# Performance work log

Measured on AMD Instinct MI355X. Metric: run time of the kernel, lower is better.

## Reference

```python
import jax, jax.numpy as jnp
import numpy as np

MIN_TEMPERATURE = 1e-8
MIN_PROB = 1e-10
NEG_INF = float('-inf')


def setup_inputs() -> dict:
    key = jax.random.key(0)
    k1, k2, k3, k4, k5 = jax.random.split(key, 5)
    B, V = 128, 128256
    logits = jax.random.normal(k1, (B, V), dtype=jnp.float32)
    temperatures = jax.random.uniform(k2, (B,), dtype=jnp.float32)
    top_ps = jax.random.uniform(k3, (B,), dtype=jnp.float32)
    top_ks = jax.random.randint(k4, (B,), 0, 1024, dtype=jnp.int64)
    min_ps = jax.random.uniform(k5, (B,), dtype=jnp.float32)
    return {"logits": logits, "temperatures": temperatures, "top_ps": top_ps,
            "top_ks": top_ks, "min_ps": min_ps}


def reference(logits, temperatures, top_ps, top_ks, min_ps):
    B, V = logits.shape
    rows = jnp.arange(B)[:, None]

    temps = jnp.maximum(temperatures, MIN_TEMPERATURE)
    original_scaled = logits.astype(jnp.float32) / temps[:, None]
    x = original_scaled

    # ---- top-k filter (rank-based; equivalent to torch.topk + scatter mask) ----
    order_k = jnp.argsort(-x, axis=-1)            # [B,V] token ids sorted desc
    ranks = jnp.argsort(order_k, axis=-1)         # rank of each token in its row
    keep_topk = ranks < top_ks[:, None]
    active_k = (top_ks > 0) & (top_ks < V)
    keep_topk = jnp.where(active_k[:, None], keep_topk, True)
    x = jnp.where(keep_topk, x, NEG_INF)

    # ---- top-p (nucleus) filter ----
    probs = jax.nn.softmax(x, axis=-1)
    order_p = jnp.argsort(-probs, axis=-1)
    sorted_probs = jnp.take_along_axis(probs, order_p, axis=-1)
    cum = jnp.cumsum(sorted_probs, axis=-1)
    remove_sorted = cum > top_ps[:, None]
    # shift right so the first token above the threshold is kept
    remove_sorted = jnp.concatenate(
        [jnp.zeros((B, 1), dtype=bool), remove_sorted[:, :-1]], axis=-1)
    remove = jnp.zeros((B, V), dtype=bool).at[rows, order_p].set(remove_sorted)
    x = jnp.where(remove, NEG_INF, x)

    # ---- min-p filter ----
    probs = jax.nn.softmax(x, axis=-1)
    top_prob = jnp.max(probs, axis=-1, keepdims=True)
    x = jnp.where(probs < min_ps[:, None] * top_prob, NEG_INF, x)

    # ---- fallback if everything got filtered ----
    all_filtered = jnp.all(jnp.isneginf(x), axis=-1)
    x = jnp.where(all_filtered[:, None], original_scaled, x)

    # ---- final softmax with nan guard + renormalize ----
    probs = jax.nn.softmax(x, axis=-1)
    probs = jnp.nan_to_num(probs, nan=0.0)
    probs = probs / jnp.maximum(jnp.sum(probs, axis=-1, keepdims=True), MIN_PROB)

    # ---- multinomial sample (1 draw per row) ----
    tokens = jax.random.categorical(jax.random.key(42), jnp.log(probs), axis=-1)
    return tokens
```

## Files before the change

kernel.cpp:

```cpp
#include <hip/hip_runtime.h>


#define TPS 512
#define TPB 1024
#define VOC 128256
#define V4 (VOC / 4)
#define NBINS 2048
#define SEG 320
#define CAPROW (8 * SEG)
#define CAP2 2048
#define TIE_CAP 1024
#define IMAXI 0x7fffffff
#define FIXS 1.7592186044416e13
#define THRK 0xC0100000u

#define WS_CNT 0
#define WS_CAP 4096

__device__ __forceinline__ unsigned fkey(float x) {
  unsigned b = __float_as_uint(x);
  return b ^ ((b & 0x80000000u) ? 0xFFFFFFFFu : 0x80000000u);
}
__device__ __forceinline__ float keyf(unsigned k) {
  unsigned b = (k & 0x80000000u) ? (k ^ 0x80000000u) : ~k;
  return __uint_as_float(b);
}
__device__ __forceinline__ unsigned rotl32(unsigned v, int r) {
  return (v << r) | (v >> (32 - r));
}

__device__ __forceinline__ float gumbel_at(unsigned i) {
  const unsigned ks1 = 42u;
  const unsigned ks2 = 0x1BD11BDAu ^ 42u;
  unsigned x0 = 0u;
  unsigned x1 = i + ks1;
  x0 += x1; x1 = rotl32(x1, 13); x1 ^= x0;
  x0 += x1; x1 = rotl32(x1, 15); x1 ^= x0;
  x0 += x1; x1 = rotl32(x1, 26); x1 ^= x0;
  x0 += x1; x1 = rotl32(x1, 6);  x1 ^= x0;
  x0 += ks1; x1 += ks2 + 1u;
  x0 += x1; x1 = rotl32(x1, 17); x1 ^= x0;
  x0 += x1; x1 = rotl32(x1, 29); x1 ^= x0;
  x0 += x1; x1 = rotl32(x1, 16); x1 ^= x0;
  x0 += x1; x1 = rotl32(x1, 24); x1 ^= x0;
  x0 += ks2; x1 += 0u + 2u;
  x0 += x1; x1 = rotl32(x1, 13); x1 ^= x0;
  x0 += x1; x1 = rotl32(x1, 15); x1 ^= x0;
  x0 += x1; x1 = rotl32(x1, 26); x1 ^= x0;
  x0 += x1; x1 = rotl32(x1, 6);  x1 ^= x0;
  x0 += 0u; x1 += ks1 + 3u;
  x0 += x1; x1 = rotl32(x1, 17); x1 ^= x0;
  x0 += x1; x1 = rotl32(x1, 29); x1 ^= x0;
  x0 += x1; x1 = rotl32(x1, 16); x1 ^= x0;
  x0 += x1; x1 = rotl32(x1, 24); x1 ^= x0;
  x0 += ks1; x1 += ks2 + 4u;
  x0 += x1; x1 = rotl32(x1, 13); x1 ^= x0;
  x0 += x1; x1 = rotl32(x1, 15); x1 ^= x0;
  x0 += x1; x1 = rotl32(x1, 26); x1 ^= x0;
  x0 += x1; x1 = rotl32(x1, 6);  x1 ^= x0;
  x0 += ks2; x1 += 0u + 5u;
  unsigned bits = x0 ^ x1;
  unsigned fb = (bits >> 9) | 0x3f800000u;
  float f = __uint_as_float(fb) - 1.0f;
  float u = (f > 0.0f) ? f : 1.17549435e-38f;
  return -logf(-logf(u));
}

__device__ __forceinline__ unsigned long long bmerge(
    unsigned long long v, int i, int size, int maxs) {
  const bool up = ((i & size) == 0);
  for (int s = maxs; s > 0; s >>= 1) {
    unsigned long long p = __shfl_xor(v, s, 64);
    bool keep_min = (up == ((i & s) == 0));
    bool take = keep_min ? (p < v) : (p > v);
    if (take) v = p;
  }
  return v;
}

__device__ __forceinline__ void scan32g(unsigned* H, int n, int tid, int tpb) {
  for (int d = 1; d < n; d <<= 1) {
    unsigned v[4]; int c = 0;
    for (int i = tid; i < n; i += tpb) {
      v[c] = H[i] + ((i + d < n) ? H[i + d] : 0u);
      ++c;
    }
    __syncthreads();
    c = 0;
    for (int i = tid; i < n; i += tpb) { H[i] = v[c]; ++c; }
    __syncthreads();
  }
}
__device__ __forceinline__ void scan64(unsigned long long* H, int n, int tid) {
  for (int d = 1; d < n; d <<= 1) {
    unsigned long long v0 = 0ull, v1 = 0ull;
    int i0 = tid, i1 = tid + TPB;
    bool a0 = (i0 < n), a1 = (i1 < n);
    if (a0) { v0 = H[i0]; if (i0 + d < n) v0 += H[i0 + d]; }
    if (a1) { v1 = H[i1]; if (i1 + d < n) v1 += H[i1 + d]; }
    __syncthreads();
    if (a0) H[i0] = v0;
    if (a1) H[i1] = v1;
    __syncthreads();
  }
}

#define FOR_ALL(...)                                                          \
  for (int c_ = 0; c_ < 32; ++c_) {                                           \
    const int i4_ = c_ * TPB + tid;                                           \
    if (i4_ < V4) {                                                           \
      const float4 L_ = ((const float4*)rowp)[i4_];                           \
      const float xs_[4] = { L_.x / tclamp, L_.y / tclamp,                    \
                             L_.z / tclamp, L_.w / tclamp };                  \
      const int base_ = i4_ * 4;                                              \
      for (int j_ = 0; j_ < 4; ++j_) {                                        \
        const int idx = base_ + j_; const float x = xs_[j_];                  \
        __VA_ARGS__                                                           \
      }                                                                       \
    }                                                                         \
  }

extern "C" __global__ void __launch_bounds__(TPS)
k3_capture(const float* __restrict__ logits, const float* __restrict__ temps,
           unsigned char* __restrict__ ws)
{
  __shared__ unsigned long long Ls[SEG];
  __shared__ unsigned sh_nloc;
  const int blk = blockIdx.x, row = blk >> 3, sb = blk & 7;
  const int tid = threadIdx.x;
  const float* rowp = logits + (size_t)row * VOC;
  const float tclamp = fmaxf(temps[row], 1e-8f);
  if (tid == 0) sh_nloc = 0u;
  __syncthreads();
  for (int c = 0; c < 8; ++c) {
    const int i4 = c * 4096 + sb * TPS + tid;
    if (i4 < V4) {
      const float4 L = ((const float4*)rowp)[i4];
      const float v[4] = { L.x, L.y, L.z, L.w };
      const int base = i4 * 4;
      for (int j = 0; j < 4; ++j) {
        if (fkey(v[j]) >= THRK) {
          float x = v[j] / tclamp;
          unsigned kx = fkey(x);
          unsigned p = atomicAdd(&sh_nloc, 1u);
          if (p < SEG)
            Ls[p] = ((unsigned long long)(~kx) << 32) | (unsigned)(base + j);
        }
      }
    }
  }
  __syncthreads();
  const unsigned nloc = sh_nloc;
  if (tid == 0) ((unsigned*)(ws + WS_CNT))[row * 8 + sb] = nloc;
  unsigned long long* cap = (unsigned long long*)(ws + WS_CAP) +
                            (size_t)row * CAPROW + (size_t)sb * SEG;
  const unsigned nw = min(nloc, (unsigned)SEG);
  for (unsigned i = tid; i < nw; i += TPS) cap[i] = Ls[i];
}

extern "C" __global__ void __launch_bounds__(TPB)
k4_sample(const float* __restrict__ logits, const float* __restrict__ temps,
          const float* __restrict__ topps, const int* __restrict__ topks,
          const float* __restrict__ minps, const unsigned char* __restrict__ ws,
          int* __restrict__ out)
{
  __shared__ unsigned long long A[CAP2];
  __shared__ unsigned Hc[NBINS];
  __shared__ double D[TPB];
  __shared__ float redw[16];
  __shared__ int   redi[16];
  __shared__ double redd[16];
  __shared__ int segoff[9];
  __shared__ int sh_bad;
  __shared__ float sh_m;
  __shared__ int sh_b0, sh_b1, sh_b2;
  __shared__ unsigned sh_above;
  __shared__ unsigned long long sh_ab64;
  __shared__ int sh_p, sh_tn, sh_I2;
  __shared__ double sh_Z3;

  const int tid = threadIdx.x;
  const int row = blockIdx.x;
  const float* rowp = logits + (size_t)row * VOC;
  const float tclamp = fmaxf(temps[row], 1e-8f);
  const float topp = topps[row];
  const float minp = minps[row];
  const int k = topks[row];
  const bool ka = (k > 0) && (k < VOC);

  if (tid == 0) {
    const unsigned* cnts = (const unsigned*)(ws + WS_CNT) + row * 8;
    int acc = 0, bad = 0;
    for (int b = 0; b < 8; ++b) {
      segoff[b] = acc;
      unsigned c = cnts[b];
      if (c > SEG) bad = 1;
      acc += (int)c;
    }
    segoff[8] = acc;
    sh_bad = bad;
  }
  __syncthreads();
  const int n = segoff[8];

  if (ka && k <= TPB && !sh_bad && n >= k && n <= CAP2) {
    const unsigned long long* capr =
        (const unsigned long long*)(ws + WS_CAP) + (size_t)row * CAPROW;
    for (int b = 0; b < 8; ++b) {
      const int off = segoff[b], cnt = segoff[b + 1] - off;
      for (int i = tid; i < cnt; i += TPB) A[off + i] = capr[b * SEG + i];
    }
    for (int i = n + tid; i < CAP2; i += TPB) A[i] = ~0ull;
    __syncthreads();
    const int lane = tid & 63, wave = tid >> 6;
    for (int g = wave; g < 32; g += 16) {
      const int i = g * 64 + lane;
      unsigned long long v = A[i];
      v = bmerge(v, i, 2, 1);
      v = bmerge(v, i, 4, 2);
      v = bmerge(v, i, 8, 4);
      v = bmerge(v, i, 16, 8);
      v = bmerge(v, i, 32, 16);
      v = bmerge(v, i, 64, 32);
      A[i] = v;
    }
    __syncthreads();
    for (int size = 128; size <= CAP2; size <<= 1) {
      for (int stride = size >> 1; stride >= 64; stride >>= 1) {
        for (int r = 0; r < 2; ++r) {
          const int i = tid + (r << 10);
          const int j = i ^ stride;
          if (j > i) {
            unsigned long long a = A[i], b = A[j];
            bool up = ((i & size) == 0);
            if ((a > b) == up) { A[i] = b; A[j] = a; }
          }
        }
        __syncthreads();
      }
      for (int g = wave; g < 32; g += 16) {
        const int i = g * 64 + lane;
        A[i] = bmerge(A[i], i, size, 32);
      }
      __syncthreads();
    }
    const float m = keyf(~(unsigned)(A[0] >> 32));
    unsigned idx_i = 0u; float e_i = 0.0f;
    const bool valid = (tid < k);
    if (valid) {
      unsigned long long a = A[tid];
      idx_i = (unsigned)a;
      e_i = expf(keyf(~(unsigned)(a >> 32)) - m);
    }
    double v = valid ? (double)e_i : 0.0;
    for (int o = 1; o < 64; o <<= 1) {
      double t = __shfl_up(v, o);
      if ((tid & 63) >= o) v += t;
    }
    if ((tid & 63) == 63) redd[tid >> 6] = v;
    __syncthreads();
    if (tid == 0) {
      double acc = 0.0;
      for (int w = 0; w < 16; ++w) { double t = redd[w]; redd[w] = acc; acc += t; }
    }
    __syncthreads();
    v += redd[tid >> 6];
    D[tid] = v;
    __syncthreads();
    const double Z1 = D[k - 1];
    const double T = (double)topp * Z1;
    if (tid == 0) sh_p = 0;
    __syncthreads();
    if (valid) {
      bool kept = (tid == 0) || (D[tid - 1] <= T);
      if (kept) atomicMax(&sh_p, tid);
    }
    __syncthreads();
    const int p2 = sh_p + 1;
    const float Z2f = (float)D[p2 - 1];
    const float e0 = expf(0.0f);
    const float thrm = minp * (e0 / Z2f);
    __syncthreads();
    if (tid == 0) sh_p = 0;
    __syncthreads();
    if (valid && tid < p2) {
      float q = e_i / Z2f;
      if (!(q < thrm)) atomicMax(&sh_p, tid);
    }
    __syncthreads();
    const int p3 = sh_p + 1;
    const float Z3f = (float)D[p3 - 1];
    float bw = -INFINITY; int bi = IMAXI;
    if (valid && tid < p3) {
      bw = logf(e_i / Z3f) + gumbel_at((unsigned)row * (unsigned)VOC + idx_i);
      bi = (int)idx_i;
    }
    for (int o = 32; o > 0; o >>= 1) {
      float ow = __shfl_down(bw, o);
      int   oi = __shfl_down(bi, o);
      if (ow > bw || (ow == bw && oi < bi)) { bw = ow; bi = oi; }
    }
    if ((tid & 63) == 0) { redw[tid >> 6] = bw; redi[tid >> 6] = bi; }
    __syncthreads();
    if (tid == 0) {
      float w = redw[0]; int ii = redi[0];
      for (int i = 1; i < 16; ++i)
        if (redw[i] > w || (redw[i] == w && redi[i] < ii)) { w = redw[i]; ii = redi[i]; }
      out[row] = ii;
    }
    return;
  }

  {
    float lmax = -INFINITY;
    FOR_ALL( (void)idx; lmax = fmaxf(lmax, x); )
    for (int o = 32; o > 0; o >>= 1) lmax = fmaxf(lmax, __shfl_down(lmax, o));
    if ((tid & 63) == 0) redw[tid >> 6] = lmax;
    __syncthreads();
    if (tid == 0) {
      float mm = redw[0];
      for (int i = 1; i < 16; ++i) mm = fmaxf(mm, redw[i]);
      sh_m = mm;
    }
    __syncthreads();
  }
  const float m = sh_m;

  unsigned tk_key = 0u; int rem_k = 0;
  if (ka) {
    for (int i = tid; i < NBINS; i += TPB) Hc[i] = 0u;
    __syncthreads();
    FOR_ALL( (void)idx; atomicAdd(&Hc[fkey(x) >> 21], 1u); )
    __syncthreads();
    scan32g(Hc, NBINS, tid, TPB);
    unsigned kku = (unsigned)k;
    for (int i = tid; i < NBINS; i += TPB) {
      unsigned hi = Hc[i], hn = (i + 1 < NBINS) ? Hc[i + 1] : 0u;
      if (hi >= kku && hn < kku) { sh_b0 = i; sh_above = hn; }
    }
    __syncthreads();
    const int b0 = sh_b0; kku -= sh_above;
    __syncthreads();
    for (int i = tid; i < NBINS; i += TPB) Hc[i] = 0u;
    __syncthreads();
    FOR_ALL(
      (void)idx;
      unsigned key = fkey(x);
      if ((int)(key >> 21) == b0) atomicAdd(&Hc[(key >> 10) & 0x7FFu], 1u);
    )
    __syncthreads();
    scan32g(Hc, NBINS, tid, TPB);
    for (int i = tid; i < NBINS; i += TPB) {
      unsigned hi = Hc[i], hn = (i + 1 < NBINS) ? Hc[i + 1] : 0u;
      if (hi >= kku && hn < kku) { sh_b1 = i; sh_above = hn; }
    }
    __syncthreads();
    const int b1 = sh_b1; kku -= sh_above;
    __syncthreads();
    for (int i = tid; i < NBINS; i += TPB) Hc[i] = 0u;
    __syncthreads();
    const unsigned pathk = ((unsigned)b0 << 11) | (unsigned)b1;
    FOR_ALL(
      (void)idx;
      unsigned key = fkey(x);
      if ((key >> 10) == pathk) atomicAdd(&Hc[key & 0x3FFu], 1u);
    )
    __syncthreads();
    scan32g(Hc, 1024, tid, TPB);
    for (int i = tid; i < 1024; i += TPB) {
      unsigned hi = Hc[i], hn = (i + 1 < 1024) ? Hc[i + 1] : 0u;
      if (hi >= kku && hn < kku) { sh_b2 = i; sh_above = hn; }
    }
    __syncthreads();
    rem_k = (int)(kku - sh_above);
    tk_key = ((unsigned)b0 << 21) | ((unsigned)b1 << 10) | (unsigned)sh_b2;
    __syncthreads();
  }
  const bool hk = ka;
  const float e_tk = hk ? expf(keyf(tk_key) - m) : 0.0f;
  const unsigned long long e_tk_fix = (unsigned long long)((double)e_tk * FIXS);
  unsigned long long* H = A;
  for (int i = tid; i < NBINS; i += TPB) H[i] = 0ull;
  __syncthreads();
  FOR_ALL(
    (void)idx;
    unsigned key = fkey(x);
    if (!hk || key > tk_key) {
      float e = expf(x - m);
      unsigned long long ef = (unsigned long long)((double)e * FIXS);
      if (ef) atomicAdd(&H[key >> 21], ef);
    }
  )
  __syncthreads();
  if (tid == 0 && hk) H[tk_key >> 21] += (unsigned long long)(unsigned)rem_k * e_tk_fix;
  __syncthreads();
  scan64(H, NBINS, tid);
  const unsigned long long Z1fix = H[0];
  const unsigned long long Tfix = (unsigned long long)((double)topp * (double)Z1fix);
  const int keepall = (Z1fix <= Tfix);

  unsigned t2_key = 0u; int rem2 = 0, all_mode = 0;
  double Z2d = 0.0; float e_t = 0.0f;

  if (!keepall) {
    for (int i = tid; i < NBINS; i += TPB) {
      unsigned long long hi = H[i], hn = (i + 1 < NBINS) ? H[i + 1] : 0ull;
      if (hi > Tfix && hn <= Tfix) { sh_b0 = i; sh_ab64 = hn; }
    }
    __syncthreads();
    const int b0p = sh_b0;
    const unsigned long long S0 = sh_ab64;
    __syncthreads();
    for (int i = tid; i < NBINS; i += TPB) H[i] = 0ull;
    __syncthreads();
    FOR_ALL(
      (void)idx;
      unsigned key = fkey(x);
      if ((int)(key >> 21) == b0p && (!hk || key > tk_key)) {
        float e = expf(x - m);
        unsigned long long ef = (unsigned long long)((double)e * FIXS);
        if (ef) atomicAdd(&H[(key >> 10) & 0x7FFu], ef);
      }
    )
    __syncthreads();
    if (tid == 0 && hk && (int)(tk_key >> 21) == b0p)
      H[(tk_key >> 10) & 0x7FFu] += (unsigned long long)(unsigned)rem_k * e_tk_fix;
    __syncthreads();
    scan64(H, NBINS, tid);
    {
      const unsigned long long T1 = Tfix - S0;
      for (int i = tid; i < NBINS; i += TPB) {
        unsigned long long hi = H[i], hn = (i + 1 < NBINS) ? H[i + 1] : 0ull;
        if (hi > T1 && hn <= T1) { sh_b1 = i; sh_ab64 = hn; }
      }
    }
    __syncthreads();
    const int b1p = sh_b1;
    const unsigned long long S1 = S0 + sh_ab64;
    __syncthreads();
    for (int i = tid; i < NBINS; i += TPB) H[i] = 0ull;
    for (int i = tid; i < 1024; i += TPB) Hc[i] = 0u;
    __syncthreads();
    const unsigned pathp = ((unsigned)b0p << 11) | (unsigned)b1p;
    FOR_ALL(
      (void)idx;
      unsigned key = fkey(x);
      if ((key >> 10) == pathp && (!hk || key > tk_key)) {
        float e = expf(x - m);
        unsigned long long ef = (unsigned long long)((double)e * FIXS);
        atomicAdd(&H[key & 0x3FFu], ef);
        atomicAdd(&Hc[key & 0x3FFu], 1u);
      }
    )
    __syncthreads();
    if (tid == 0 && hk && (tk_key >> 10) == pathp) {
      H[tk_key & 0x3FFu] += (unsigned long long)(unsigned)rem_k * e_tk_fix;
      Hc[tk_key & 0x3FFu] += (unsigned)rem_k;
    }
    __syncthreads();
    scan64(H, 1024, tid);
    {
      const unsigned long long T2 = Tfix - S1;
      for (int i = tid; i < 1024; i += TPB) {
        unsigned long long hi = H[i], hn = (i + 1 < 1024) ? H[i + 1] : 0ull;
        if (hi > T2 && hn <= T2) { sh_b2 = i; sh_ab64 = hn; }
      }
    }
    __syncthreads();
    const int b2p = sh_b2;
    const unsigned long long Sfix = S1 + sh_ab64;
    t2_key = ((unsigned)b0p << 21) | ((unsigned)b1p << 10) | (unsigned)b2p;
    const int c_t2 = (int)Hc[b2p];
    e_t = expf(keyf(t2_key) - m);
    const double Td = (double)topp * ((double)Z1fix / FIXS);
    const double Sd = (double)Sfix / FIXS;
    const double jmd = (Td - Sd) / (double)e_t;
    int rem_p;
    if (jmd >= (double)c_t2) rem_p = c_t2;
    else {
      rem_p = (int)jmd + 1;
      if (rem_p > c_t2) rem_p = c_t2;
      if (rem_p < 1) rem_p = 1;
    }
    rem2 = rem_p;
    const unsigned long long Z2fix =
        Sfix + (unsigned long long)(unsigned)rem_p *
                   (unsigned long long)((double)e_t * FIXS);
    Z2d = (double)Z2fix / FIXS;
  } else {
    if (hk) { t2_key = tk_key; rem2 = rem_k; e_t = e_tk; }
    else    { all_mode = 1; }
    Z2d = (double)Z1fix / FIXS;
  }

  if (tid == 0) { sh_tn = 0; sh_I2 = IMAXI; }
  __syncthreads();
  const float Z2f = (float)Z2d;
  const float thrm = minp * (1.0f / Z2f);
  double zp = 0.0;
  FOR_ALL(
    unsigned key = fkey(x);
    if (all_mode || key > t2_key) {
      float e = expf(x - m);
      float q1 = e / Z2f;
      if (!(q1 < thrm)) zp += (double)e;
    } else if (key == t2_key) {
      int p = atomicAdd(&sh_tn, 1);
      if (p < TIE_CAP) Hc[p] = (unsigned)idx;
    }
  )
  for (int o = 32; o > 0; o >>= 1) zp += __shfl_down(zp, o);
  if ((tid & 63) == 0) redd[tid >> 6] = zp;
  __syncthreads();
  int class_ok = 1;
  if (!all_mode) { float q1t = e_t / Z2f; class_ok = !(q1t < thrm); }
  if (tid == 0) {
    double z3 = 0.0;
    for (int i = 0; i < 16; ++i) z3 += redd[i];
    if (!all_mode && class_ok) z3 += (double)rem2 * (double)e_t;
    sh_Z3 = z3;
  }
  __syncthreads();
  const int tn = sh_tn;
  if (!all_mode && rem2 < tn && tn <= TIE_CAP) {
    if (tid < tn) {
      unsigned mine = Hc[tid];
      int r = 0;
      for (int j = 0; j < tn; ++j) r += (Hc[j] < mine);
      if (r == rem2 - 1) sh_I2 = (int)mine;
    }
  }
  __syncthreads();
  const int I2 = sh_I2;
  const float Z3f = (float)sh_Z3;
  float bw = -INFINITY; int bi = IMAXI;
  FOR_ALL(
    unsigned key = fkey(x);
    bool kp = all_mode || key > t2_key || (key == t2_key && idx <= I2);
    if (kp) {
      float e = expf(x - m);
      float q1 = e / Z2f;
      if (!(q1 < thrm)) {
        float w = logf(e / Z3f) + gumbel_at((unsigned)row * (unsigned)VOC + (unsigned)idx);
        if (w > bw) { bw = w; bi = idx; }
        else if (w == bw && idx < bi) bi = idx;
      }
    }
  )
  for (int o = 32; o > 0; o >>= 1) {
    float ow = __shfl_down(bw, o);
    int   oi = __shfl_down(bi, o);
    if (ow > bw || (ow == bw && oi < bi)) { bw = ow; bi = oi; }
  }
  if ((tid & 63) == 0) { redw[tid >> 6] = bw; redi[tid >> 6] = bi; }
  __syncthreads();
  if (tid == 0) {
    float w = redw[0]; int ii = redi[0];
    for (int i = 1; i < 16; ++i)
      if (redw[i] > w || (redw[i] == w && redi[i] < ii)) { w = redw[i]; ii = redi[i]; }
    out[row] = ii;
  }
}

extern "C" void kernel_launch(void* const* d_in, const int* in_sizes, int n_in,
                              void* d_out, int out_size, void* d_ws, size_t ws_size,
                              hipStream_t stream) {
  (void)n_in; (void)ws_size; (void)out_size;
  const float* logits = (const float*)d_in[0];
  const float* temps  = (const float*)d_in[1];
  const float* topps  = (const float*)d_in[2];
  const int*   topks  = (const int*)d_in[3];
  const float* minps  = (const float*)d_in[4];
  int* out = (int*)d_out;
  const int rows = in_sizes[1];
  unsigned char* ws = (unsigned char*)d_ws;
  k3_capture<<<dim3(rows * 8), dim3(TPS), 0, stream>>>(logits, temps, ws);
  k4_sample<<<dim3(rows), dim3(TPB), 0, stream>>>(logits, temps, topps, topks,
                                                  minps, ws, out);
}
```

Baseline: 125.9 us.

## Fuse capture and sample kernels using last-block-done atomic counter per row

Merges the two-kernel pipeline into one kernel. Each row is now split across 4 blocks of 1024 threads instead of 8 blocks of 512, and the last block to finish a row, found through a per-row atomic counter after a threadfence, goes on to the sampling phase. This removes one kernel launch boundary and lets sampling for early rows overlap with capture for other rows. In exchange it adds a memset launch, a larger shared-memory footprint for every block (which lowers occupancy during capture), and fewer capture blocks.

```diff
diff --git a/kernel.cpp b/kernel.cpp
--- a/kernel.cpp
+++ b/kernel.cpp
@@ -1,21 +1,22 @@
 #include <hip/hip_runtime.h>
 
 
-#define TPS 512
 #define TPB 1024
 #define VOC 128256
 #define V4 (VOC / 4)
+#define Q4 (V4 / 4)
 #define NBINS 2048
-#define SEG 320
-#define CAPROW (8 * SEG)
+#define SEG 640
+#define CAPROW (4 * SEG)
 #define CAP2 2048
 #define TIE_CAP 1024
 #define IMAXI 0x7fffffff
 #define FIXS 1.7592186044416e13
 #define THRK 0xC0100000u
 
-#define WS_CNT 0
-#define WS_CAP 4096
+#define WS_DONE 0
+#define WS_CNT  512
+#define WS_CAP  4096
 
 __device__ __forceinline__ unsigned fkey(float x) {
   unsigned b = __float_as_uint(x);
@@ -120,21 +121,42 @@
     }                                                                         \
   }
 
-extern "C" __global__ void __launch_bounds__(TPS)
-k3_capture(const float* __restrict__ logits, const float* __restrict__ temps,
-           unsigned char* __restrict__ ws)
+extern "C" __global__ void __launch_bounds__(TPB)
+sampler_fused(const float* __restrict__ logits, const float* __restrict__ temps,
+              const float* __restrict__ topps, const int* __restrict__ topks,
+              const float* __restrict__ minps, unsigned char* __restrict__ ws,
+              int* __restrict__ out)
 {
   __shared__ unsigned long long Ls[SEG];
+  __shared__ unsigned long long A[CAP2];
+  __shared__ unsigned Hc[NBINS];
+  __shared__ double D[TPB];
+  __shared__ float redw[16];
+  __shared__ int   redi[16];
+  __shared__ double redd[16];
   __shared__ unsigned sh_nloc;
-  const int blk = blockIdx.x, row = blk >> 3, sb = blk & 7;
+  __shared__ int sh_last;
+  __shared__ int segoff[5];
+  __shared__ int sh_bad;
+  __shared__ float sh_m;
+  __shared__ int sh_b0, sh_b1, sh_b2;
+  __shared__ unsigned sh_above;
+  __shared__ unsigned long long sh_ab64;
+  __shared__ int sh_p, sh_tn, sh_I2;
+  __shared__ double sh_Z3;
+
+  const int blk = blockIdx.x;
+  const int row = blk >> 2, sb = blk & 3;
   const int tid = threadIdx.x;
   const float* rowp = logits + (size_t)row * VOC;
   const float tclamp = fmaxf(temps[row], 1e-8f);
+
   if (tid == 0) sh_nloc = 0u;
   __syncthreads();
   for (int c = 0; c < 8; ++c) {
-    const int i4 = c * 4096 + sb * TPS + tid;
-    if (i4 < V4) {
+    const int t = c * TPB + tid;
+    if (t < Q4) {
+      const int i4 = sb * Q4 + t;
       const float4 L = ((const float4*)rowp)[i4];
       const float v[4] = { L.x, L.y, L.z, L.w };
       const int base = i4 * 4;
@@ -151,62 +173,46 @@
   }
   __syncthreads();
   const unsigned nloc = sh_nloc;
-  if (tid == 0) ((unsigned*)(ws + WS_CNT))[row * 8 + sb] = nloc;
-  unsigned long long* cap = (unsigned long long*)(ws + WS_CAP) +
-                            (size_t)row * CAPROW + (size_t)sb * SEG;
-  const unsigned nw = min(nloc, (unsigned)SEG);
-  for (unsigned i = tid; i < nw; i += TPS) cap[i] = Ls[i];
-}
-
-extern "C" __global__ void __launch_bounds__(TPB)
-k4_sample(const float* __restrict__ logits, const float* __restrict__ temps,
-          const float* __restrict__ topps, const int* __restrict__ topks,
-          const float* __restrict__ minps, const unsigned char* __restrict__ ws,
-          int* __restrict__ out)
-{
-  __shared__ unsigned long long A[CAP2];
-  __shared__ unsigned Hc[NBINS];
-  __shared__ double D[TPB];
-  __shared__ float redw[16];
-  __shared__ int   redi[16];
-  __shared__ double redd[16];
-  __shared__ int segoff[9];
-  __shared__ int sh_bad;
-  __shared__ float sh_m;
-  __shared__ int sh_b0, sh_b1, sh_b2;
-  __shared__ unsigned sh_above;
-  __shared__ unsigned long long sh_ab64;
-  __shared__ int sh_p, sh_tn, sh_I2;
-  __shared__ double sh_Z3;
-
-  const int tid = threadIdx.x;
-  const int row = blockIdx.x;
-  const float* rowp = logits + (size_t)row * VOC;
-  const float tclamp = fmaxf(temps[row], 1e-8f);
+  if (tid == 0) ((unsigned*)(ws + WS_CNT))[row * 4 + sb] = nloc;
+  {
+    unsigned long long* cap = (unsigned long long*)(ws + WS_CAP) +
+                              (size_t)row * CAPROW + (size_t)sb * SEG;
+    const unsigned nw = min(nloc, (unsigned)SEG);
+    for (unsigned i = tid; i < nw; i += TPB) cap[i] = Ls[i];
+  }
+  __threadfence();
+  if (tid == 0) {
+    unsigned old = atomicAdd(&((unsigned*)(ws + WS_DONE))[row], 1u);
+    sh_last = (old == 3u);
+  }
+  __syncthreads();
+  if (!sh_last) return;
+  __threadfence();
+
   const float topp = topps[row];
   const float minp = minps[row];
   const int k = topks[row];
   const bool ka = (k > 0) && (k < VOC);
 
   if (tid == 0) {
-    const unsigned* cnts = (const unsigned*)(ws + WS_CNT) + row * 8;
+    const unsigned* cnts = (const unsigned*)(ws + WS_CNT) + row * 4;
     int acc = 0, bad = 0;
-    for (int b = 0; b < 8; ++b) {
+    for (int b = 0; b < 4; ++b) {
       segoff[b] = acc;
       unsigned c = cnts[b];
       if (c > SEG) bad = 1;
       acc += (int)c;
     }
-    segoff[8] = acc;
+    segoff[4] = acc;
     sh_bad = bad;
   }
   __syncthreads();
-  const int n = segoff[8];
+  const int n = segoff[4];
 
   if (ka && k <= TPB && !sh_bad && n >= k && n <= CAP2) {
     const unsigned long long* capr =
         (const unsigned long long*)(ws + WS_CAP) + (size_t)row * CAPROW;
-    for (int b = 0; b < 8; ++b) {
+    for (int b = 0; b < 4; ++b) {
       const int off = segoff[b], cnt = segoff[b + 1] - off;
       for (int i = tid; i < cnt; i += TPB) A[off + i] = capr[b * SEG + i];
     }
@@ -574,7 +580,7 @@
   int* out = (int*)d_out;
   const int rows = in_sizes[1];
   unsigned char* ws = (unsigned char*)d_ws;
-  k3_capture<<<dim3(rows * 8), dim3(TPS), 0, stream>>>(logits, temps, ws);
-  k4_sample<<<dim3(rows), dim3(TPB), 0, stream>>>(logits, temps, topps, topks,
-                                                  minps, ws, out);
-}
+  hipMemsetAsync(ws + WS_DONE, 0, rows * sizeof(unsigned), stream);
+  sampler_fused<<<dim3(rows * 4), dim3(TPB), 0, stream>>>(
+      logits, temps, topps, topks, minps, ws, out);
+}
```

Result: slower. 350.0 us (+178.1%).
